# Kernel tuning notes

Measured on AMD Instinct MI355X. Metric: run time of the kernel, lower is better.

## Reference

```python
import jax, jax.numpy as jnp
import numpy as np
import math

B, S, D = 4, 1024, 1024
NH, HD = 16, 64
I = 4096
EPS = 1e-12


def layer_norm(x, g, b):
    mu = jnp.mean(x, axis=-1, keepdims=True)
    var = jnp.mean((x - mu) ** 2, axis=-1, keepdims=True)
    return (x - mu) * jax.lax.rsqrt(var + EPS) * g + b


def setup_inputs() -> dict:
    key = jax.random.key(0)
    ks = jax.random.split(key, 12)
    s = 0.02
    return {
        "hidden_states": jax.random.normal(ks[0], (B, S, D), jnp.float32),
        "attention_mask": jnp.zeros((B, 1, 1, S), jnp.float32),
        "Wq": jax.random.normal(ks[1], (D, D), jnp.float32) * s,
        "bq": jnp.zeros((D,), jnp.float32),
        "Wk": jax.random.normal(ks[2], (D, D), jnp.float32) * s,
        "bk": jnp.zeros((D,), jnp.float32),
        "Wv": jax.random.normal(ks[3], (D, D), jnp.float32) * s,
        "bv": jnp.zeros((D,), jnp.float32),
        "Wo": jax.random.normal(ks[4], (D, D), jnp.float32) * s,
        "bo": jnp.zeros((D,), jnp.float32),
        "ln1_g": jnp.ones((D,), jnp.float32),
        "ln1_b": jnp.zeros((D,), jnp.float32),
        "Wi": jax.random.normal(ks[5], (D, I), jnp.float32) * s,
        "bi": jnp.zeros((I,), jnp.float32),
        "Wout": jax.random.normal(ks[6], (I, D), jnp.float32) * s,
        "bout": jnp.zeros((D,), jnp.float32),
        "ln2_g": jnp.ones((D,), jnp.float32),
        "ln2_b": jnp.zeros((D,), jnp.float32),
    }


def reference(hidden_states, attention_mask, Wq, bq, Wk, bk, Wv, bv, Wo, bo,
              ln1_g, ln1_b, Wi, bi, Wout, bout, ln2_g, ln2_b):
    h = hidden_states
    # QKV projections, split into heads: [B,S,D] -> [B,NH,S,HD]
    def heads(x):
        return x.reshape(B, S, NH, HD).transpose(0, 2, 1, 3)
    q = heads(h @ Wq + bq)
    k = heads(h @ Wk + bk)
    v = heads(h @ Wv + bv)
    # manual attention: scores [B,NH,S,S]
    scores = jnp.einsum("bhqd,bhkd->bhqk", q, k) / math.sqrt(HD)
    scores = scores + attention_mask
    probs = jax.nn.softmax(scores, axis=-1)
    ctx = jnp.einsum("bhqk,bhkd->bhqd", probs, v)
    ctx = ctx.transpose(0, 2, 1, 3).reshape(B, S, D)
    # self-output: dense + residual + LN
    attn_out = layer_norm(ctx @ Wo + bo + h, ln1_g, ln1_b)
    # FFN: dense + exact gelu, dense + residual + LN
    inter = jax.nn.gelu(attn_out @ Wi + bi, approximate=False)
    out = layer_norm(inter @ Wout + bout + attn_out, ln2_g, ln2_b)
    return out
```

## Files before the change

kernel.cpp:

```cpp
#include <hip/hip_runtime.h>
#include <hip/hip_bf16.h>
#include <math.h>

#define B_ 4
#define S_ 1024
#define D_ 1024
#define NH_ 16
#define HD_ 64
#define I_ 4096
#define M_ (B_*S_)

typedef __bf16 bf16_8 __attribute__((ext_vector_type(8)));
typedef float f32x4 __attribute__((ext_vector_type(4)));
typedef unsigned int u32x2 __attribute__((ext_vector_type(2)));
typedef unsigned short u16;

struct PB { u16* p[4]; };
struct Prep {
    const float* s[6]; u16* d[6]; int K[6]; int N[6];
    const float4* cin; ushort4* cout;
};

__device__ __forceinline__ u16 f2b(float x) {
    __hip_bfloat16 h = __float2bfloat16(x);
    return *reinterpret_cast<u16*>(&h);
}
__device__ __forceinline__ float b2f(u16 x) {
    return __uint_as_float(((unsigned)x) << 16);
}

__device__ __forceinline__ void gload16(const void* g, void* l) {
    __builtin_amdgcn_global_load_lds(
        (const __attribute__((address_space(1))) void*)g,
        (__attribute__((address_space(3))) void*)l, 16, 0, 0);
}

__device__ __forceinline__ float gelu_f(float v) {
    const float z  = v * 0.70710678118654752f;
    const float az = fabsf(z);
    const float t  = __fdividef(1.0f, 1.0f + 0.3275911f * az);
    const float poly = t * (0.254829592f + t * (-0.284496736f +
                       t * (1.421413741f + t * (-1.453152027f + t * 1.061405429f))));
    const float erfa = 1.0f - poly * __expf(-z * z);
    const float erfv = copysignf(erfa, z);
    return 0.5f * v * (1.0f + erfv);
}

__global__ __launch_bounds__(256) void prep_all(Prep p)
{
    const int tid = threadIdx.x;
    const int z = blockIdx.z;
    const int tile = blockIdx.y * 128 + blockIdx.x;

    if (z == 6) {
        const int i = tile * 256 + tid;
        float4 v = p.cin[i];
        ushort4 o;
        o.x = f2b(v.x); o.y = f2b(v.y); o.z = f2b(v.z); o.w = f2b(v.w);
        p.cout[i] = o;
        return;
    }

    const int K = p.K[z], N = p.N[z];
    const int ntile = N >> 5;
    if (tile >= (K >> 5) * ntile) return;
    const int k0 = (tile / ntile) * 32, n0 = (tile % ntile) * 32;
    const float* in = p.s[z];
    u16* out = p.d[z];

    __shared__ float t[32][33];
#pragma unroll
    for (int i = 0; i < 4; ++i) {
        int idx = i * 256 + tid;
        int r = idx >> 5, c = idx & 31;
        t[r][c] = in[(size_t)(k0 + r) * N + n0 + c];
    }
    __syncthreads();
    const int rr = tid >> 3, cc0 = (tid & 7) * 4;
    ushort4 o;
    o.x = f2b(t[cc0 + 0][rr]);
    o.y = f2b(t[cc0 + 1][rr]);
    o.z = f2b(t[cc0 + 2][rr]);
    o.w = f2b(t[cc0 + 3][rr]);
    *(ushort4*)(out + (size_t)(n0 + rr) * K + k0 + cc0) = o;
}

#define NT_ 16

template<int MODE>
__global__ __launch_bounds__(512, 2) void gemm256(
    const u16* __restrict__ A, const u16* __restrict__ Bt,
    const float* __restrict__ b0, const float* __restrict__ b1,
    const float* __restrict__ b2,
    u16* __restrict__ outB, PB parts, int N, int sA, int sB)
{
    __shared__ __align__(16) char sm[131072];

    const int tid  = threadIdx.x;
    const int lane = tid & 63, wid = tid >> 6;
    const int l15  = lane & 15, lg = lane >> 4;
    const int gm   = wid >> 2, gn = wid & 3;
    const int bm   = blockIdx.y * 256, bn = blockIdx.x * 256;
    const int koff = (MODE == 2) ? blockIdx.z * 1024 : 0;

    const int srow = (wid << 3) + (lane >> 3);
    const int skb  = ((lane & 7) << 4) ^ (((lane >> 3) & 7) << 4);
    const int scol = skb >> 1;
    const int xm   = (l15 & 7) << 4;

    f32x4 acc[8][4];
#pragma unroll
    for (int m = 0; m < 8; ++m)
#pragma unroll
        for (int j = 0; j < 4; ++j) {
            acc[m][j][0] = 0.f; acc[m][j][1] = 0.f;
            acc[m][j][2] = 0.f; acc[m][j][3] = 0.f;
        }

    auto stageA = [&](int v, int h) {
        const u16* src = A + (size_t)(bm + h * 128 + srow) * sA + koff + v * 64 + scol;
        char* dst = sm + ((v & 1) * 65536 + h * 16384 + wid * 1024);
        gload16(src, dst);
        gload16(src + (size_t)64 * sA, dst + 8192);
    };
    auto stageB = [&](int v, int h) {
        const u16* src = Bt + (size_t)(bn + h * 128 + srow) * sB + koff + v * 64 + scol;
        char* dst = sm + ((v & 1) * 65536 + 32768 + h * 16384 + wid * 1024);
        gload16(src, dst);
        gload16(src + (size_t)64 * sB, dst + 8192);
    };

    bf16_8 a[8], bb[2];
    auto loadA = [&](int vb, int s) {
        const char* base = sm + (vb * 65536 + gm * 16384);
#pragma unroll
        for (int m = 0; m < 8; ++m)
            a[m] = *(const bf16_8*)(base + (m * 16 + l15) * 128 +
                                    ((s * 64 + lg * 16) ^ xm));
    };
    auto loadB = [&](int vb, int s, int np) {
        const char* base = sm + (vb * 65536 + 32768 + (gn >> 1) * 16384);
#pragma unroll
        for (int j = 0; j < 2; ++j)
            bb[j] = *(const bf16_8*)(base + ((gn & 1) * 64 + (np * 2 + j) * 16 + l15) * 128 +
                                     ((s * 64 + lg * 16) ^ xm));
    };
    auto mfma16 = [&](int np) {
#pragma unroll
        for (int m = 0; m < 8; ++m)
#pragma unroll
            for (int j = 0; j < 2; ++j)
                acc[m][np * 2 + j] = __builtin_amdgcn_mfma_f32_16x16x32_bf16(
                    a[m], bb[j], acc[m][np * 2 + j], 0, 0, 0);
    };

    stageA(0, 0); stageA(0, 1);
    stageB(0, 0); stageB(0, 1);
    stageA(1, 0); stageA(1, 1);
    asm volatile("s_waitcnt vmcnt(4)" ::: "memory");
    __builtin_amdgcn_sched_barrier(0);
    __builtin_amdgcn_s_barrier();

    for (int v = 0; v < NT_ - 2; ++v) {
        const int vb = v & 1;
        loadA(vb, 0); loadB(vb, 0, 0);
        stageB(v + 1, 0); stageB(v + 1, 1);
        __builtin_amdgcn_s_barrier();
        asm volatile("s_waitcnt lgkmcnt(0)" ::: "memory");
        __builtin_amdgcn_s_setprio(1); mfma16(0); __builtin_amdgcn_s_setprio(0);
        __builtin_amdgcn_s_barrier();
        loadB(vb, 0, 1);
        __builtin_amdgcn_s_barrier();
        asm volatile("s_waitcnt lgkmcnt(0)" ::: "memory");
        __builtin_amdgcn_s_setprio(1); mfma16(1); __builtin_amdgcn_s_setprio(0);
        __builtin_amdgcn_s_barrier();
        loadA(vb, 1); loadB(vb, 1, 0);
        __builtin_amdgcn_s_barrier();
        asm volatile("s_waitcnt lgkmcnt(0)" ::: "memory");
        __builtin_amdgcn_s_setprio(1); mfma16(0); __builtin_amdgcn_s_setprio(0);
        __builtin_amdgcn_s_barrier();
        loadB(vb, 1, 1);
        stageA(v + 2, 0); stageA(v + 2, 1);
        __builtin_amdgcn_s_barrier();
        asm volatile("s_waitcnt lgkmcnt(0)" ::: "memory");
        __builtin_amdgcn_s_setprio(1); mfma16(1); __builtin_amdgcn_s_setprio(0);
        asm volatile("s_waitcnt vmcnt(4)" ::: "memory");
        __builtin_amdgcn_sched_barrier(0);
        __builtin_amdgcn_s_barrier();
    }
    {
        const int vb = (NT_ - 2) & 1;
        loadA(vb, 0); loadB(vb, 0, 0);
        stageB(NT_ - 1, 0); stageB(NT_ - 1, 1);
        __builtin_amdgcn_s_barrier();
        asm volatile("s_waitcnt lgkmcnt(0)" ::: "memory");
        __builtin_amdgcn_s_setprio(1); mfma16(0); __builtin_amdgcn_s_setprio(0);
        __builtin_amdgcn_s_barrier();
        loadB(vb, 0, 1);
        __builtin_amdgcn_s_barrier();
        asm volatile("s_waitcnt lgkmcnt(0)" ::: "memory");
        __builtin_amdgcn_s_setprio(1); mfma16(1); __builtin_amdgcn_s_setprio(0);
        __builtin_amdgcn_s_barrier();
        loadA(vb, 1); loadB(vb, 1, 0);
        __builtin_amdgcn_s_barrier();
        asm volatile("s_waitcnt lgkmcnt(0)" ::: "memory");
        __builtin_amdgcn_s_setprio(1); mfma16(0); __builtin_amdgcn_s_setprio(0);
        __builtin_amdgcn_s_barrier();
        loadB(vb, 1, 1);
        __builtin_amdgcn_s_barrier();
        asm volatile("s_waitcnt lgkmcnt(0)" ::: "memory");
        __builtin_amdgcn_s_setprio(1); mfma16(1); __builtin_amdgcn_s_setprio(0);
        asm volatile("s_waitcnt vmcnt(0)" ::: "memory");
        __builtin_amdgcn_sched_barrier(0);
        __builtin_amdgcn_s_barrier();
    }
    {
        const int vb = (NT_ - 1) & 1;
        loadA(vb, 0); loadB(vb, 0, 0); mfma16(0);
        loadB(vb, 0, 1);               mfma16(1);
        loadA(vb, 1); loadB(vb, 1, 0); mfma16(0);
        loadB(vb, 1, 1);               mfma16(1);
    }

    if (MODE == 2) {
        u16* oP = parts.p[blockIdx.z];
#pragma unroll
        for (int m = 0; m < 8; ++m)
#pragma unroll
            for (int r = 0; r < 4; ++r) {
                const int row = bm + gm * 128 + m * 16 + lg * 4 + r;
#pragma unroll
                for (int j = 0; j < 4; ++j)
                    oP[(size_t)row * N + bn + gn * 64 + j * 16 + l15] = f2b(acc[m][j][r]);
            }
    } else {
        const int cg = (bn + gn * 64) >> 10;
        const float* bp = (MODE == 0) ? (cg == 0 ? b0 : cg == 1 ? b1 : b2) : b0;
        const int cbase = (MODE == 0) ? ((bn + gn * 64) & 1023) : (bn + gn * 64);
        float bs[4];
#pragma unroll
        for (int j = 0; j < 4; ++j) bs[j] = bp[cbase + j * 16 + l15];
#pragma unroll
        for (int m = 0; m < 8; ++m)
#pragma unroll
            for (int r = 0; r < 4; ++r) {
                const int row = bm + gm * 128 + m * 16 + lg * 4 + r;
#pragma unroll
                for (int j = 0; j < 4; ++j) {
                    float v = acc[m][j][r] + bs[j];
                    if (MODE == 1) v = gelu_f(v);
                    outB[(size_t)row * N + bn + gn * 64 + j * 16 + l15] = f2b(v);
                }
            }
    }
}

__global__ __launch_bounds__(256) void gemm_splitk(
    const u16* __restrict__ A, const u16* __restrict__ Bt,
    PB parts, int N, int K, int kchunk)
{
    __shared__ __align__(16) u16 As[128 * 32];
    __shared__ __align__(16) u16 Bs[128 * 32];

    const int tid  = threadIdx.x;
    const int lane = tid & 63, wid = tid >> 6;
    const int l15  = lane & 15, lg = lane >> 4;
    const int wm   = (wid >> 1) * 64, wn = (wid & 1) * 64;
    const int bm   = blockIdx.y * 128, bn = blockIdx.x * 128;
    const int wbase16 = (tid & ~63) * 16;
    const int kt0 = blockIdx.z * kchunk, kt1 = kt0 + kchunk;
    u16* outP = parts.p[blockIdx.z];

    const int r0 = tid >> 2;
    const int c0 = (tid & 3) * 8;

    f32x4 acc[4][4];
#pragma unroll
    for (int i = 0; i < 4; ++i)
#pragma unroll
        for (int j = 0; j < 4; ++j) {
            acc[i][j][0] = 0.f; acc[i][j][1] = 0.f;
            acc[i][j][2] = 0.f; acc[i][j][3] = 0.f;
        }

    for (int kt = kt0; kt < kt1; kt += 32) {
        __syncthreads();
        gload16(A  + (size_t)(bm + r0)      * K + kt + c0, (char*)As + wbase16);
        gload16(A  + (size_t)(bm + r0 + 64) * K + kt + c0, (char*)As + wbase16 + 4096);
        gload16(Bt + (size_t)(bn + r0)      * K + kt + c0, (char*)Bs + wbase16);
        gload16(Bt + (size_t)(bn + r0 + 64) * K + kt + c0, (char*)Bs + wbase16 + 4096);
        __syncthreads();

        bf16_8 af[4], bfr[4];
#pragma unroll
        for (int f = 0; f < 4; ++f) {
            af[f]  = *(const bf16_8*)((const char*)As + (wm + f * 16 + l15) * 64 + lg * 16);
            bfr[f] = *(const bf16_8*)((const char*)Bs + (wn + f * 16 + l15) * 64 + lg * 16);
        }
#pragma unroll
        for (int i = 0; i < 4; ++i)
#pragma unroll
            for (int j = 0; j < 4; ++j)
                acc[i][j] = __builtin_amdgcn_mfma_f32_16x16x32_bf16(
                    af[i], bfr[j], acc[i][j], 0, 0, 0);
    }

#pragma unroll
    for (int i = 0; i < 4; ++i)
#pragma unroll
        for (int r = 0; r < 4; ++r) {
            const int row = bm + wm + i * 16 + lg * 4 + r;
#pragma unroll
            for (int j = 0; j < 4; ++j)
                outP[(size_t)row * N + bn + wn + j * 16 + l15] = f2b(acc[i][j][r]);
        }
}

template<int NPART>
__global__ __launch_bounds__(256) void ln_reduce(
    PB parts, const float* __restrict__ bias, const float* __restrict__ res,
    const float* __restrict__ g, const float* __restrict__ b,
    float* __restrict__ O, u16* __restrict__ OB)
{
    const int row = blockIdx.x;
    const int tid = threadIdx.x;
    const size_t off = (size_t)row * D_ + tid * 4;

    float4 v = *(const float4*)(res + off);
    const float4 bi = *(const float4*)(bias + tid * 4);
    v.x += bi.x; v.y += bi.y; v.z += bi.z; v.w += bi.w;
#pragma unroll
    for (int p = 0; p < NPART; ++p) {
        const ushort4 t = *(const ushort4*)(parts.p[p] + off);
        v.x += b2f(t.x); v.y += b2f(t.y); v.z += b2f(t.z); v.w += b2f(t.w);
    }

    float s  = v.x + v.y + v.z + v.w;
    float sq = v.x * v.x + v.y * v.y + v.z * v.z + v.w * v.w;
#pragma unroll
    for (int o = 32; o; o >>= 1) {
        s  += __shfl_down(s, o);
        sq += __shfl_down(sq, o);
    }
    __shared__ float red[8];
    const int wid = tid >> 6, lane = tid & 63;
    if (lane == 0) { red[wid] = s; red[4 + wid] = sq; }
    __syncthreads();
    const float ts = red[0] + red[1] + red[2] + red[3];
    const float tq = red[4] + red[5] + red[6] + red[7];
    const float mu  = ts * (1.0f / D_);
    const float var = tq * (1.0f / D_) - mu * mu;
    const float rs  = rsqrtf(var + 1e-12f);

    const float4 gv = *(const float4*)(g + tid * 4);
    const float4 bv = *(const float4*)(b + tid * 4);
    float4 o;
    o.x = (v.x - mu) * rs * gv.x + bv.x;
    o.y = (v.y - mu) * rs * gv.y + bv.y;
    o.z = (v.z - mu) * rs * gv.z + bv.z;
    o.w = (v.w - mu) * rs * gv.w + bv.w;
    *(float4*)(O + off) = o;
    if (OB) {
        ushort4 ob;
        ob.x = f2b(o.x); ob.y = f2b(o.y); ob.z = f2b(o.z); ob.w = f2b(o.w);
        *(ushort4*)(OB + off) = ob;
    }
}

__global__ __launch_bounds__(512) void attn_mfma(
    const u16* __restrict__ Qb, const u16* __restrict__ Kb,
    const u16* __restrict__ Vb, const float* __restrict__ mask,
    u16* __restrict__ ctxb, int qs)
{
    __shared__ __align__(16) char sm[32768];
    char* Ksm = sm;
    char* Vsm = sm + 8192;

    const int tid  = threadIdx.x;
    const int lane = tid & 63, wid = tid >> 6;
    char* Psm = sm + 16384 + wid * 2048;
    const int l15 = lane & 15, lg = lane >> 4;

    const int wg  = blockIdx.x;
    const int swz = (wg & 7) * 64 + (wg >> 3);
    const int b   = swz >> 7;
    const int h   = (swz >> 3) & 15;
    const int qb  = swz & 7;

    const int q0 = qb * 128 + wid * 16;
    const size_t inhead  = ((size_t)b * S_) * qs + (size_t)h * 64;
    const size_t outhead = ((size_t)b * S_) * D_ + (size_t)h * 64;

    const u16* Qrow = Qb + inhead + (size_t)(q0 + l15) * qs;
    const bf16_8 qf0 = *(const bf16_8*)(Qrow + lg * 8);
    const bf16_8 qf1 = *(const bf16_8*)(Qrow + 32 + lg * 8);

    f32x4 ctx[4];
#pragma unroll
    for (int i = 0; i < 4; ++i) { ctx[i][0]=0.f; ctx[i][1]=0.f; ctx[i][2]=0.f; ctx[i][3]=0.f; }
    float m_r = -1e30f, l_r = 0.f;

    const int skey = tid >> 3;
    const int sd0  = (tid & 7) * 8;
    const int xo_p = (l15 & 7) << 4;
    const int kwoff = skey * 128 + ((sd0 * 2) ^ ((skey & 7) << 4));
    const int vwoff = (sd0 >> 4) * 2048 + skey * 32 + ((sd0 & 8) << 1);

    const __attribute__((address_space(3))) char* vtr =
        (const __attribute__((address_space(3))) char*)(Vsm + lg * 256 + l15 * 2);

    bf16_8 kreg = *(const bf16_8*)(Kb + inhead + (size_t)skey * qs + sd0);
    bf16_8 vreg = *(const bf16_8*)(Vb + inhead + (size_t)skey * qs + sd0);

    for (int t = 0; t < S_ / 64; ++t) {
        __syncthreads();
        *(bf16_8*)(Ksm + kwoff) = kreg;
        *(bf16_8*)(Vsm + vwoff) = vreg;
        __syncthreads();
        if (t < S_ / 64 - 1) {
            const size_t noff = inhead + (size_t)((t + 1) * 64 + skey) * qs + sd0;
            kreg = *(const bf16_8*)(Kb + noff);
            vreg = *(const bf16_8*)(Vb + noff);
        }

        f32x4 sc[4];
#pragma unroll
        for (int kf = 0; kf < 4; ++kf) {
            const int key = kf * 16 + l15;
            f32x4 a; a[0]=0.f; a[1]=0.f; a[2]=0.f; a[3]=0.f;
            const bf16_8 kA = *(const bf16_8*)(Ksm + key * 128 + ((lg * 16)      ^ xo_p));
            a = __builtin_amdgcn_mfma_f32_16x16x32_bf16(kA, qf0, a, 0, 0, 0);
            const bf16_8 kB = *(const bf16_8*)(Ksm + key * 128 + ((64 + lg * 16) ^ xo_p));
            a = __builtin_amdgcn_mfma_f32_16x16x32_bf16(kB, qf1, a, 0, 0, 0);
            sc[kf] = a;
        }

        float p[16];
        float tmax = -1e30f;
#pragma unroll
        for (int kf = 0; kf < 4; ++kf) {
            const float4 mk = *(const float4*)(mask + (size_t)b * S_ + t * 64 + kf * 16 + lg * 4);
#pragma unroll
            for (int r = 0; r < 4; ++r) {
                const float mkr = (r == 0) ? mk.x : (r == 1) ? mk.y : (r == 2) ? mk.z : mk.w;
                p[kf * 4 + r] = sc[kf][r] * 0.125f + mkr;
                tmax = fmaxf(tmax, p[kf * 4 + r]);
            }
        }
        tmax = fmaxf(tmax, __shfl_xor(tmax, 16));
        tmax = fmaxf(tmax, __shfl_xor(tmax, 32));

        const float mnew = fmaxf(m_r, tmax);
        const float scl  = __expf(m_r - mnew);
        m_r = mnew;

        float psum = 0.f;
#pragma unroll
        for (int i = 0; i < 16; ++i) {
            p[i] = __expf(p[i] - mnew);
            psum += p[i];
        }
        psum += __shfl_xor(psum, 16);
        psum += __shfl_xor(psum, 32);
        l_r = l_r * scl + psum;

#pragma unroll
        for (int fd = 0; fd < 4; ++fd)
#pragma unroll
            for (int r = 0; r < 4; ++r) ctx[fd][r] *= scl;

#pragma unroll
        for (int kf = 0; kf < 4; ++kf)
#pragma unroll
            for (int rr = 0; rr < 2; ++rr) {
                ushort2 wv;
                wv.x = f2b(p[kf * 4 + 2 * rr]);
                wv.y = f2b(p[kf * 4 + 2 * rr + 1]);
                *(ushort2*)(Psm + l15 * 128 +
                            (((kf * 16 + lg * 4 + 2 * rr) * 2) ^ xo_p)) = wv;
            }
        asm volatile("s_waitcnt lgkmcnt(0)" ::: "memory");

#pragma unroll
        for (int s = 0; s < 2; ++s) {
            const bf16_8 pf = *(const bf16_8*)(Psm + l15 * 128 +
                                ((s * 64 + lg * 16) ^ xo_p));
            const __attribute__((address_space(3))) char* a3 = vtr + s * 1024;
            u32x2 r0, r1, r2, r3, r4, r5, r6, r7;
            asm volatile(
                "ds_read_b64_tr_b16 %0, %8 offset:0\n\t"
                "ds_read_b64_tr_b16 %1, %8 offset:128\n\t"
                "ds_read_b64_tr_b16 %2, %8 offset:2048\n\t"
                "ds_read_b64_tr_b16 %3, %8 offset:2176\n\t"
                "ds_read_b64_tr_b16 %4, %8 offset:4096\n\t"
                "ds_read_b64_tr_b16 %5, %8 offset:4224\n\t"
                "ds_read_b64_tr_b16 %6, %8 offset:6144\n\t"
                "ds_read_b64_tr_b16 %7, %8 offset:6272\n\t"
                "s_waitcnt lgkmcnt(0)"
                : "=&v"(r0), "=&v"(r1), "=&v"(r2), "=&v"(r3),
                  "=&v"(r4), "=&v"(r5), "=&v"(r6), "=&v"(r7)
                : "v"(a3));
            union Cv { unsigned u[4]; bf16_8 v; };
            Cv c0; c0.u[0] = r0.x; c0.u[1] = r0.y; c0.u[2] = r1.x; c0.u[3] = r1.y;
            Cv c1; c1.u[0] = r2.x; c1.u[1] = r2.y; c1.u[2] = r3.x; c1.u[3] = r3.y;
            Cv c2; c2.u[0] = r4.x; c2.u[1] = r4.y; c2.u[2] = r5.x; c2.u[3] = r5.y;
            Cv c3; c3.u[0] = r6.x; c3.u[1] = r6.y; c3.u[2] = r7.x; c3.u[3] = r7.y;
            ctx[0] = __builtin_amdgcn_mfma_f32_16x16x32_bf16(c0.v, pf, ctx[0], 0, 0, 0);
            ctx[1] = __builtin_amdgcn_mfma_f32_16x16x32_bf16(c1.v, pf, ctx[1], 0, 0, 0);
            ctx[2] = __builtin_amdgcn_mfma_f32_16x16x32_bf16(c2.v, pf, ctx[2], 0, 0, 0);
            ctx[3] = __builtin_amdgcn_mfma_f32_16x16x32_bf16(c3.v, pf, ctx[3], 0, 0, 0);
        }
    }

    const float inv = 1.f / l_r;
    const size_t qrow = outhead + (size_t)(q0 + l15) * D_;
#pragma unroll
    for (int fd = 0; fd < 4; ++fd) {
        ushort4 o;
        o.x = f2b(ctx[fd][0] * inv);
        o.y = f2b(ctx[fd][1] * inv);
        o.z = f2b(ctx[fd][2] * inv);
        o.w = f2b(ctx[fd][3] * inv);
        *(ushort4*)(ctxb + qrow + fd * 16 + lg * 4) = o;
    }
}

extern "C" void kernel_launch(void* const* d_in, const int* in_sizes, int n_in,
                              void* d_out, int out_size, void* d_ws, size_t ws_size,
                              hipStream_t stream)
{
    const float* h    = (const float*)d_in[0];
    const float* mask = (const float*)d_in[1];
    const float* Wq   = (const float*)d_in[2];
    const float* bq   = (const float*)d_in[3];
    const float* Wk   = (const float*)d_in[4];
    const float* bk   = (const float*)d_in[5];
    const float* Wv   = (const float*)d_in[6];
    const float* bv   = (const float*)d_in[7];
    const float* Wo   = (const float*)d_in[8];
    const float* bo   = (const float*)d_in[9];
    const float* ln1g = (const float*)d_in[10];
    const float* ln1b = (const float*)d_in[11];
    const float* Wi   = (const float*)d_in[12];
    const float* bi   = (const float*)d_in[13];
    const float* Wout = (const float*)d_in[14];
    const float* bout = (const float*)d_in[15];
    const float* ln2g = (const float*)d_in[16];
    const float* ln2b = (const float*)d_in[17];
    float* out = (float*)d_out;

    char* w = (char*)d_ws;
    const size_t MiB = 1ull << 20;
    u16*   Woutt  = (u16*)(w + 0);
    u16*   Wit    = (u16*)(w + 8 * MiB);
    u16*   hb     = (u16*)(w + 16 * MiB);
    u16*   woP0   = (u16*)(w + 16 * MiB);
    u16*   ffP1   = (u16*)(w + 16 * MiB);
    u16*   Wqkvt  = (u16*)(w + 24 * MiB);
    u16*   ffP2   = (u16*)(w + 24 * MiB);
    u16*   Wot    = (u16*)(w + 30 * MiB);
    u16*   QKVb   = (u16*)(w + 32 * MiB);
    u16*   woP1   = (u16*)(w + 32 * MiB);
    u16*   ffP3   = (u16*)(w + 32 * MiB);
    float* attnF  = (float*)(w + 40 * MiB);
    u16*   attnB  = (u16*)(w + 56 * MiB);
    u16*   interB = (u16*)(w + 64 * MiB);
    u16*   ctxb   = (u16*)(w + 96 * MiB);
    u16*   ffP0   = (u16*)(w + 96 * MiB);

    const dim3 blk(256);
    PB zp; zp.p[0] = zp.p[1] = zp.p[2] = zp.p[3] = nullptr;

    Prep pp;
    pp.s[0] = Wq;   pp.d[0] = Wqkvt;                 pp.K[0] = D_; pp.N[0] = D_;
    pp.s[1] = Wk;   pp.d[1] = Wqkvt + 1024 * 1024;   pp.K[1] = D_; pp.N[1] = D_;
    pp.s[2] = Wv;   pp.d[2] = Wqkvt + 2 * 1024 * 1024; pp.K[2] = D_; pp.N[2] = D_;
    pp.s[3] = Wo;   pp.d[3] = Wot;                   pp.K[3] = D_; pp.N[3] = D_;
    pp.s[4] = Wi;   pp.d[4] = Wit;                   pp.K[4] = D_; pp.N[4] = I_;
    pp.s[5] = Wout; pp.d[5] = Woutt;                 pp.K[5] = I_; pp.N[5] = D_;
    pp.cin  = (const float4*)h;
    pp.cout = (ushort4*)hb;
    prep_all<<<dim3(128, 32, 7), blk, 0, stream>>>(pp);

    gemm256<0><<<dim3(12, 16, 1), dim3(512), 0, stream>>>(
        hb, Wqkvt, bq, bk, bv, QKVb, zp, 3072, 1024, 1024);

    attn_mfma<<<dim3(512), dim3(512), 0, stream>>>(
        QKVb, QKVb + 1024, QKVb + 2048, mask, ctxb, 3072);

    PB woP; woP.p[0] = woP0; woP.p[1] = woP1; woP.p[2] = nullptr; woP.p[3] = nullptr;
    gemm_splitk<<<dim3(8, 32, 2), blk, 0, stream>>>(ctxb, Wot, woP, D_, D_, 512);
    ln_reduce<2><<<dim3(M_), blk, 0, stream>>>(woP, bo, h, ln1g, ln1b, attnF, attnB);

    gemm256<1><<<dim3(16, 16, 1), dim3(512), 0, stream>>>(
        attnB, Wit, bi, nullptr, nullptr, interB, zp, 4096, 1024, 1024);

    PB ffP; ffP.p[0] = ffP0; ffP.p[1] = ffP1; ffP.p[2] = ffP2; ffP.p[3] = ffP3;
    gemm256<2><<<dim3(4, 16, 4), dim3(512), 0, stream>>>(
        interB, Woutt, nullptr, nullptr, nullptr, nullptr, ffP, 1024, 4096, 4096);
    ln_reduce<4><<<dim3(M_), blk, 0, stream>>>(ffP, bout, attnF, ln2g, ln2b, out, nullptr);
}
```

Before: 210.9 us.

## Replace FFN-out split-K4 GEMM with 256x128 tile split-K2 triple-buffered kernel

The FFN output GEMM moves to a dedicated kernel with 256x128 tiles, split-K of 2 instead of 4, and a three-stage LDS ring buffer that prefetches two K-steps ahead. The grid stays at 256 blocks, but each block now covers half the N width and twice the K depth. This cuts the partial-sum traffic and the final layer-norm reduction to two partials, and the deeper buffering aims to hide global load latency. In exchange it uses more LDS (144KB), which may limit occupancy, and fewer accumulators per wave lowers arithmetic intensity per LDS read.

After: 219.4 us. 1.04x slower.

```diff
diff --git a/kernel.cpp b/kernel.cpp
--- a/kernel.cpp
+++ b/kernel.cpp
@@ -92,7 +92,7 @@
     const u16* __restrict__ A, const u16* __restrict__ Bt,
     const float* __restrict__ b0, const float* __restrict__ b1,
     const float* __restrict__ b2,
-    u16* __restrict__ outB, PB parts, int N, int sA, int sB)
+    u16* __restrict__ outB, int N, int sA, int sB)
 {
     __shared__ __align__(16) char sm[131072];
 
@@ -101,7 +101,6 @@
     const int l15  = lane & 15, lg = lane >> 4;
     const int gm   = wid >> 2, gn = wid & 3;
     const int bm   = blockIdx.y * 256, bn = blockIdx.x * 256;
-    const int koff = (MODE == 2) ? blockIdx.z * 1024 : 0;
 
     const int srow = (wid << 3) + (lane >> 3);
     const int skb  = ((lane & 7) << 4) ^ (((lane >> 3) & 7) << 4);
@@ -118,13 +117,13 @@
         }
 
     auto stageA = [&](int v, int h) {
-        const u16* src = A + (size_t)(bm + h * 128 + srow) * sA + koff + v * 64 + scol;
+        const u16* src = A + (size_t)(bm + h * 128 + srow) * sA + v * 64 + scol;
         char* dst = sm + ((v & 1) * 65536 + h * 16384 + wid * 1024);
         gload16(src, dst);
         gload16(src + (size_t)64 * sA, dst + 8192);
     };
     auto stageB = [&](int v, int h) {
-        const u16* src = Bt + (size_t)(bn + h * 128 + srow) * sB + koff + v * 64 + scol;
+        const u16* src = Bt + (size_t)(bn + h * 128 + srow) * sB + v * 64 + scol;
         char* dst = sm + ((v & 1) * 65536 + 32768 + h * 16384 + wid * 1024);
         gload16(src, dst);
         gload16(src + (size_t)64 * sB, dst + 8192);
@@ -222,18 +221,7 @@
         loadB(vb, 1, 1);               mfma16(1);
     }
 
-    if (MODE == 2) {
-        u16* oP = parts.p[blockIdx.z];
-#pragma unroll
-        for (int m = 0; m < 8; ++m)
-#pragma unroll
-            for (int r = 0; r < 4; ++r) {
-                const int row = bm + gm * 128 + m * 16 + lg * 4 + r;
-#pragma unroll
-                for (int j = 0; j < 4; ++j)
-                    oP[(size_t)row * N + bn + gn * 64 + j * 16 + l15] = f2b(acc[m][j][r]);
-            }
-    } else {
+    {
         const int cg = (bn + gn * 64) >> 10;
         const float* bp = (MODE == 0) ? (cg == 0 ? b0 : cg == 1 ? b1 : b2) : b0;
         const int cbase = (MODE == 0) ? ((bn + gn * 64) & 1023) : (bn + gn * 64);
@@ -253,6 +241,128 @@
                 }
             }
     }
+}
+
+#define NTS_ 32
+
+__global__ __launch_bounds__(512, 2) void gemm256_skn(
+    const u16* __restrict__ A, const u16* __restrict__ Bt, PB parts)
+{
+    __shared__ __align__(16) char sm[147456];
+
+    const int tid  = threadIdx.x;
+    const int lane = tid & 63, wid = tid >> 6;
+    const int l15  = lane & 15, lg = lane >> 4;
+    const int gm   = wid >> 2, gn = wid & 3;
+    const int bm   = blockIdx.y * 256, bn = blockIdx.x * 128;
+    const int koff = blockIdx.z * 2048;
+
+    const int srow = (wid << 3) + (lane >> 3);
+    const int skb  = ((lane & 7) << 4) ^ (((lane >> 3) & 7) << 4);
+    const int scol = skb >> 1;
+    const int xm   = (l15 & 7) << 4;
+
+    f32x4 acc[8][2];
+#pragma unroll
+    for (int m = 0; m < 8; ++m)
+#pragma unroll
+        for (int j = 0; j < 2; ++j) {
+            acc[m][j][0] = 0.f; acc[m][j][1] = 0.f;
+            acc[m][j][2] = 0.f; acc[m][j][3] = 0.f;
+        }
+
+    auto stageA = [&](int v, int h, int base) {
+        const u16* src = A + (size_t)(bm + h * 128 + srow) * 4096 + koff + v * 64 + scol;
+        char* dst = sm + base + h * 16384 + wid * 1024;
+        gload16(src, dst);
+        gload16(src + (size_t)64 * 4096, dst + 8192);
+    };
+    auto stageB = [&](int v, int base) {
+        const u16* src = Bt + (size_t)(bn + srow) * 4096 + koff + v * 64 + scol;
+        char* dst = sm + base + 32768 + wid * 1024;
+        gload16(src, dst);
+        gload16(src + (size_t)64 * 4096, dst + 8192);
+    };
+
+    bf16_8 a[8], bb[2];
+    auto loadA = [&](int base, int s) {
+        const char* bp = sm + base + gm * 16384;
+#pragma unroll
+        for (int m = 0; m < 8; ++m)
+            a[m] = *(const bf16_8*)(bp + (m * 16 + l15) * 128 +
+                                    ((s * 64 + lg * 16) ^ xm));
+    };
+    auto loadB = [&](int base, int s) {
+        const char* bp = sm + base + 32768;
+#pragma unroll
+        for (int j = 0; j < 2; ++j)
+            bb[j] = *(const bf16_8*)(bp + (gn * 32 + j * 16 + l15) * 128 +
+                                     ((s * 64 + lg * 16) ^ xm));
+    };
+    auto mfma16 = [&]() {
+#pragma unroll
+        for (int m = 0; m < 8; ++m)
+#pragma unroll
+            for (int j = 0; j < 2; ++j)
+                acc[m][j] = __builtin_amdgcn_mfma_f32_16x16x32_bf16(
+                    a[m], bb[j], acc[m][j], 0, 0, 0);
+    };
+
+    int a0 = 0, a1 = 49152, a2 = 98304;
+
+    stageB(0, a0); stageA(0, 0, a0); stageA(0, 1, a0);
+    stageB(1, a1); stageA(1, 0, a1); stageA(1, 1, a1);
+    asm volatile("s_waitcnt vmcnt(6)" ::: "memory");
+    __builtin_amdgcn_sched_barrier(0);
+    __builtin_amdgcn_s_barrier();
+
+    for (int v = 0; v < NTS_ - 2; ++v) {
+        loadA(a0, 0); loadB(a0, 0);
+        stageB(v + 2, a2);
+        __builtin_amdgcn_s_barrier();
+        asm volatile("s_waitcnt lgkmcnt(0)" ::: "memory");
+        __builtin_amdgcn_s_setprio(1); mfma16(); __builtin_amdgcn_s_setprio(0);
+        __builtin_amdgcn_s_barrier();
+        loadA(a0, 1); loadB(a0, 1);
+        stageA(v + 2, 0, a2); stageA(v + 2, 1, a2);
+        __builtin_amdgcn_s_barrier();
+        asm volatile("s_waitcnt lgkmcnt(0)" ::: "memory");
+        __builtin_amdgcn_s_setprio(1); mfma16(); __builtin_amdgcn_s_setprio(0);
+        asm volatile("s_waitcnt vmcnt(6)" ::: "memory");
+        __builtin_amdgcn_sched_barrier(0);
+        __builtin_amdgcn_s_barrier();
+        const int t = a0; a0 = a1; a1 = a2; a2 = t;
+    }
+    {
+        loadA(a0, 0); loadB(a0, 0);
+        __builtin_amdgcn_s_barrier();
+        asm volatile("s_waitcnt lgkmcnt(0)" ::: "memory");
+        __builtin_amdgcn_s_setprio(1); mfma16(); __builtin_amdgcn_s_setprio(0);
+        __builtin_amdgcn_s_barrier();
+        loadA(a0, 1); loadB(a0, 1);
+        __builtin_amdgcn_s_barrier();
+        asm volatile("s_waitcnt lgkmcnt(0)" ::: "memory");
+        __builtin_amdgcn_s_setprio(1); mfma16(); __builtin_amdgcn_s_setprio(0);
+        asm volatile("s_waitcnt vmcnt(0)" ::: "memory");
+        __builtin_amdgcn_sched_barrier(0);
+        __builtin_amdgcn_s_barrier();
+        const int t = a0; a0 = a1; a1 = a2; a2 = t;
+    }
+    {
+        loadA(a0, 0); loadB(a0, 0); mfma16();
+        loadA(a0, 1); loadB(a0, 1); mfma16();
+    }
+
+    u16* oP = parts.p[blockIdx.z];
+#pragma unroll
+    for (int m = 0; m < 8; ++m)
+#pragma unroll
+        for (int r = 0; r < 4; ++r) {
+            const int row = bm + gm * 128 + m * 16 + lg * 4 + r;
+#pragma unroll
+            for (int j = 0; j < 2; ++j)
+                oP[(size_t)row * 1024 + bn + gn * 32 + j * 16 + l15] = f2b(acc[m][j][r]);
+        }
 }
 
 __global__ __launch_bounds__(256) void gemm_splitk(
@@ -557,11 +667,9 @@
     u16*   woP0   = (u16*)(w + 16 * MiB);
     u16*   ffP1   = (u16*)(w + 16 * MiB);
     u16*   Wqkvt  = (u16*)(w + 24 * MiB);
-    u16*   ffP2   = (u16*)(w + 24 * MiB);
     u16*   Wot    = (u16*)(w + 30 * MiB);
     u16*   QKVb   = (u16*)(w + 32 * MiB);
     u16*   woP1   = (u16*)(w + 32 * MiB);
-    u16*   ffP3   = (u16*)(w + 32 * MiB);
     float* attnF  = (float*)(w + 40 * MiB);
     u16*   attnB  = (u16*)(w + 56 * MiB);
     u16*   interB = (u16*)(w + 64 * MiB);
@@ -569,7 +677,6 @@
     u16*   ffP0   = (u16*)(w + 96 * MiB);
 
     const dim3 blk(256);
-    PB zp; zp.p[0] = zp.p[1] = zp.p[2] = zp.p[3] = nullptr;
 
     Prep pp;
     pp.s[0] = Wq;   pp.d[0] = Wqkvt;                 pp.K[0] = D_; pp.N[0] = D_;
@@ -583,7 +690,7 @@
     prep_all<<<dim3(128, 32, 7), blk, 0, stream>>>(pp);
 
     gemm256<0><<<dim3(12, 16, 1), dim3(512), 0, stream>>>(
-        hb, Wqkvt, bq, bk, bv, QKVb, zp, 3072, 1024, 1024);
+        hb, Wqkvt, bq, bk, bv, QKVb, 3072, 1024, 1024);
 
     attn_mfma<<<dim3(512), dim3(512), 0, stream>>>(
         QKVb, QKVb + 1024, QKVb + 2048, mask, ctxb, 3072);
@@ -593,10 +700,9 @@
     ln_reduce<2><<<dim3(M_), blk, 0, stream>>>(woP, bo, h, ln1g, ln1b, attnF, attnB);
 
     gemm256<1><<<dim3(16, 16, 1), dim3(512), 0, stream>>>(
-        attnB, Wit, bi, nullptr, nullptr, interB, zp, 4096, 1024, 1024);
-
-    PB ffP; ffP.p[0] = ffP0; ffP.p[1] = ffP1; ffP.p[2] = ffP2; ffP.p[3] = ffP3;
-    gemm256<2><<<dim3(4, 16, 4), dim3(512), 0, stream>>>(
-        interB, Woutt, nullptr, nullptr, nullptr, nullptr, ffP, 1024, 4096, 4096);
-    ln_reduce<4><<<dim3(M_), blk, 0, stream>>>(ffP, bout, attnF, ln2g, ln2b, out, nullptr);
-}
+        attnB, Wit, bi, nullptr, nullptr, interB, 4096, 1024, 1024);
+
+    PB ffP; ffP.p[0] = ffP0; ffP.p[1] = ffP1; ffP.p[2] = nullptr; ffP.p[3] = nullptr;
+    gemm256_skn<<<dim3(8, 16, 2), dim3(512), 0, stream>>>(interB, Woutt, ffP);
+    ln_reduce<2><<<dim3(M_), blk, 0, stream>>>(ffP, bout, attnF, ln2g, ln2b, out, nullptr);
+}
```

## Halve attention workgroup size and add lazy online-softmax rescaling

Applied to the files above, without the earlier changes.

The attention kernel now uses 256-thread workgroups with 64 query rows each, launching 1024 workgroups instead of 512. Each thread stages two K and two V rows per tile, and the block-to-(batch, head, qblock) mapping is reordered. The online softmax now rescales the accumulators and the running sum only when some lane's tile max exceeds the running max by more than 8. This skips the exp and the multiplies on most tiles, at the cost of bounded growth in the unnormalized values. Smaller workgroups may improve occupancy and load balance, but every block streams the full K/V per head, so K/V loads double.

Result: slower. 231.6 us (+9.8%).

```diff
diff --git a/kernel.cpp b/kernel.cpp
--- a/kernel.cpp
+++ b/kernel.cpp
@@ -367,12 +367,12 @@
     }
 }
 
-__global__ __launch_bounds__(512) void attn_mfma(
+__global__ __launch_bounds__(256) void attn_mfma(
     const u16* __restrict__ Qb, const u16* __restrict__ Kb,
     const u16* __restrict__ Vb, const float* __restrict__ mask,
     u16* __restrict__ ctxb, int qs)
 {
-    __shared__ __align__(16) char sm[32768];
+    __shared__ __align__(16) char sm[24576];
     char* Ksm = sm;
     char* Vsm = sm + 8192;
 
@@ -381,13 +381,13 @@
     char* Psm = sm + 16384 + wid * 2048;
     const int l15 = lane & 15, lg = lane >> 4;
 
-    const int wg  = blockIdx.x;
-    const int swz = (wg & 7) * 64 + (wg >> 3);
-    const int b   = swz >> 7;
-    const int h   = (swz >> 3) & 15;
-    const int qb  = swz & 7;
-
-    const int q0 = qb * 128 + wid * 16;
+    const int wg = blockIdx.x;
+    const int g  = (wg & 7) + 8 * ((wg >> 3) & 7);
+    const int qb = wg >> 6;
+    const int b  = g >> 4;
+    const int h  = g & 15;
+
+    const int q0 = qb * 64 + wid * 16;
     const size_t inhead  = ((size_t)b * S_) * qs + (size_t)h * 64;
     const size_t outhead = ((size_t)b * S_) * D_ + (size_t)h * 64;
 
@@ -400,27 +400,36 @@
     for (int i = 0; i < 4; ++i) { ctx[i][0]=0.f; ctx[i][1]=0.f; ctx[i][2]=0.f; ctx[i][3]=0.f; }
     float m_r = -1e30f, l_r = 0.f;
 
-    const int skey = tid >> 3;
-    const int sd0  = (tid & 7) * 8;
+    const int sk0 = tid >> 3;
+    const int sk1 = sk0 + 32;
+    const int sd0 = (tid & 7) * 8;
     const int xo_p = (l15 & 7) << 4;
-    const int kwoff = skey * 128 + ((sd0 * 2) ^ ((skey & 7) << 4));
-    const int vwoff = (sd0 >> 4) * 2048 + skey * 32 + ((sd0 & 8) << 1);
+    const int kw0 = sk0 * 128 + ((sd0 * 2) ^ ((sk0 & 7) << 4));
+    const int kw1 = sk1 * 128 + ((sd0 * 2) ^ ((sk1 & 7) << 4));
+    const int vw0 = (sd0 >> 4) * 2048 + sk0 * 32 + ((sd0 & 8) << 1);
+    const int vw1 = (sd0 >> 4) * 2048 + sk1 * 32 + ((sd0 & 8) << 1);
 
     const __attribute__((address_space(3))) char* vtr =
         (const __attribute__((address_space(3))) char*)(Vsm + lg * 256 + l15 * 2);
 
-    bf16_8 kreg = *(const bf16_8*)(Kb + inhead + (size_t)skey * qs + sd0);
-    bf16_8 vreg = *(const bf16_8*)(Vb + inhead + (size_t)skey * qs + sd0);
+    bf16_8 kreg0 = *(const bf16_8*)(Kb + inhead + (size_t)sk0 * qs + sd0);
+    bf16_8 kreg1 = *(const bf16_8*)(Kb + inhead + (size_t)sk1 * qs + sd0);
+    bf16_8 vreg0 = *(const bf16_8*)(Vb + inhead + (size_t)sk0 * qs + sd0);
+    bf16_8 vreg1 = *(const bf16_8*)(Vb + inhead + (size_t)sk1 * qs + sd0);
 
     for (int t = 0; t < S_ / 64; ++t) {
         __syncthreads();
-        *(bf16_8*)(Ksm + kwoff) = kreg;
-        *(bf16_8*)(Vsm + vwoff) = vreg;
+        *(bf16_8*)(Ksm + kw0) = kreg0;
+        *(bf16_8*)(Ksm + kw1) = kreg1;
+        *(bf16_8*)(Vsm + vw0) = vreg0;
+        *(bf16_8*)(Vsm + vw1) = vreg1;
         __syncthreads();
         if (t < S_ / 64 - 1) {
-            const size_t noff = inhead + (size_t)((t + 1) * 64 + skey) * qs + sd0;
-            kreg = *(const bf16_8*)(Kb + noff);
-            vreg = *(const bf16_8*)(Vb + noff);
+            const size_t base = inhead + (size_t)((t + 1) * 64) * qs + sd0;
+            kreg0 = *(const bf16_8*)(Kb + base + (size_t)sk0 * qs);
+            kreg1 = *(const bf16_8*)(Kb + base + (size_t)sk1 * qs);
+            vreg0 = *(const bf16_8*)(Vb + base + (size_t)sk0 * qs);
+            vreg1 = *(const bf16_8*)(Vb + base + (size_t)sk1 * qs);
         }
 
         f32x4 sc[4];
@@ -450,24 +459,26 @@
         tmax = fmaxf(tmax, __shfl_xor(tmax, 16));
         tmax = fmaxf(tmax, __shfl_xor(tmax, 32));
 
-        const float mnew = fmaxf(m_r, tmax);
-        const float scl  = __expf(m_r - mnew);
-        m_r = mnew;
+        if (!__all(tmax <= m_r + 8.0f)) {
+            const float mnew = fmaxf(m_r, tmax);
+            const float scl  = __expf(m_r - mnew);
+            m_r = mnew;
+            l_r *= scl;
+#pragma unroll
+            for (int fd = 0; fd < 4; ++fd)
+#pragma unroll
+                for (int r = 0; r < 4; ++r) ctx[fd][r] *= scl;
+        }
 
         float psum = 0.f;
 #pragma unroll
         for (int i = 0; i < 16; ++i) {
-            p[i] = __expf(p[i] - mnew);
+            p[i] = __expf(p[i] - m_r);
             psum += p[i];
         }
         psum += __shfl_xor(psum, 16);
         psum += __shfl_xor(psum, 32);
-        l_r = l_r * scl + psum;
-
-#pragma unroll
-        for (int fd = 0; fd < 4; ++fd)
-#pragma unroll
-            for (int r = 0; r < 4; ++r) ctx[fd][r] *= scl;
+        l_r += psum;
 
 #pragma unroll
         for (int kf = 0; kf < 4; ++kf)
@@ -585,7 +596,7 @@
     gemm256<0><<<dim3(12, 16, 1), dim3(512), 0, stream>>>(
         hb, Wqkvt, bq, bk, bv, QKVb, zp, 3072, 1024, 1024);
 
-    attn_mfma<<<dim3(512), dim3(512), 0, stream>>>(
+    attn_mfma<<<dim3(1024), dim3(256), 0, stream>>>(
         QKVb, QKVb + 1024, QKVb + 2048, mask, ctxb, 3072);
 
     PB woP; woP.p[0] = woP0; woP.p[1] = woP1; woP.p[2] = nullptr; woP.p[3] = nullptr;
```
